# Kernel tuning notes

Measured on AMD Instinct MI355X. Metric: run time of the kernel, lower is better.

The kernel has to match this reference:

```python
import jax, jax.numpy as jnp
import numpy as np

D_MODEL = 1024
HEADS = 16
D_K = D_MODEL // HEADS


def setup_inputs() -> dict:
    key = jax.random.key(0)
    ks = jax.random.split(key, 12)
    B, S = 2, 2048
    scale = 1.0 / np.sqrt(D_MODEL)
    inp = {
        "q": jax.random.normal(ks[0], (B, S, D_MODEL), dtype=jnp.float32),
        "k": jax.random.normal(ks[1], (B, S, D_MODEL), dtype=jnp.float32),
        "v": jax.random.normal(ks[2], (B, S, D_MODEL), dtype=jnp.float32),
        "src_mask": jax.random.randint(ks[3], (B, 1, S), 0, 2, dtype=jnp.int32),
        # projection params (nn.Linear: y = x @ W.T + b); store W already transposed
        "Wq": jax.random.normal(ks[4], (D_MODEL, D_MODEL), dtype=jnp.float32) * scale,
        "bq": jnp.zeros((D_MODEL,), dtype=jnp.float32),
        "Wk": jax.random.normal(ks[5], (D_MODEL, D_MODEL), dtype=jnp.float32) * scale,
        "bk": jnp.zeros((D_MODEL,), dtype=jnp.float32),
        "Wv": jax.random.normal(ks[6], (D_MODEL, D_MODEL), dtype=jnp.float32) * scale,
        "bv": jnp.zeros((D_MODEL,), dtype=jnp.float32),
        "Wo": jax.random.normal(ks[7], (D_MODEL, D_MODEL), dtype=jnp.float32) * scale,
        "bo": jnp.zeros((D_MODEL,), dtype=jnp.float32),
    }
    return inp


def reference(q, k, v, src_mask, Wq, bq, Wk, bk, Wv, bv, Wo, bo):
    B, S, _ = q.shape
    # QKV projections, reshape to (b, heads, seq, d_k)
    def proj(x, W, b):
        y = x @ W + b  # (b, s, d_model)
        return y.reshape(B, S, HEADS, D_K).transpose(0, 2, 1, 3)

    qh = proj(q, Wq, bq)
    kh = proj(k, Wk, bk)
    vh = proj(v, Wv, bv)

    # scaled dot-product attention with padding mask
    scores = jnp.einsum("bhqd,bhkd->bhqk", qh, kh) / jnp.sqrt(jnp.float32(D_K))
    mask = src_mask[:, None, :, :]  # (b,1,1,s), broadcast over heads & query
    scores = jnp.where(mask == 0, jnp.float32(-1e9), scores)
    probs = jax.nn.softmax(scores, axis=-1)
    # dropout is identity in eval mode (reference baseline)
    ctx = jnp.einsum("bhqk,bhkd->bhqd", probs, vh)
    ctx = ctx.transpose(0, 2, 1, 3).reshape(B, S, D_MODEL)
    return ctx @ Wo + bo
```

## Files before the change

### kernel.cpp

```cpp
#include <hip/hip_runtime.h>
#include <hip/hip_bf16.h>

#define DM 1024
#define SL 2048
#define NH 16
#define DK 64

typedef __bf16 bf16;
typedef __bf16 bf16x8 __attribute__((ext_vector_type(8)));
typedef __bf16 bf16x4 __attribute__((ext_vector_type(4)));
typedef float f32x4 __attribute__((ext_vector_type(4)));
typedef float f32x16 __attribute__((ext_vector_type(16)));
typedef unsigned u32x4 __attribute__((ext_vector_type(4)));

__device__ __forceinline__ void gll16(const void* g, void* l) {
  __builtin_amdgcn_global_load_lds(
      (const __attribute__((address_space(1))) unsigned int*)g,
      (__attribute__((address_space(3))) unsigned int*)l, 16, 0, 0);
}

__device__ __forceinline__ unsigned pk2(float a, float b) {
  unsigned short lo = __builtin_bit_cast(unsigned short, (bf16)a);
  unsigned short hi = __builtin_bit_cast(unsigned short, (bf16)b);
  return (unsigned)lo | ((unsigned)hi << 16);
}

__global__ __launch_bounds__(256) void cvt_x_kernel(
    const float* __restrict__ q, const float* __restrict__ k, const float* __restrict__ v,
    bf16* __restrict__ xq, bf16* __restrict__ xk, bf16* __restrict__ xv) {
  const float* src; bf16* dst;
  if (blockIdx.y == 0)      { src = q; dst = xq; }
  else if (blockIdx.y == 1) { src = k; dst = xk; }
  else                      { src = v; dst = xv; }
  int i = (blockIdx.x * 256 + threadIdx.x) * 8;
  f32x4 a = *(const f32x4*)(src + i);
  f32x4 b = *(const f32x4*)(src + i + 4);
  bf16x8 o;
  o[0]=(bf16)a[0]; o[1]=(bf16)a[1]; o[2]=(bf16)a[2]; o[3]=(bf16)a[3];
  o[4]=(bf16)b[0]; o[5]=(bf16)b[1]; o[6]=(bf16)b[2]; o[7]=(bf16)b[3];
  *(bf16x8*)(dst + i) = o;
}

__global__ __launch_bounds__(256) void cvt_w_kernel(
    const float* __restrict__ W0, const float* __restrict__ W1,
    const float* __restrict__ W2, const float* __restrict__ W3,
    bf16* __restrict__ T0, bf16* __restrict__ T1,
    bf16* __restrict__ T2, bf16* __restrict__ T3) {
  const float* W; bf16* T;
  switch (blockIdx.y) {
    case 0:  W = W0; T = T0; break;
    case 1:  W = W1; T = T1; break;
    case 2:  W = W2; T = T2; break;
    default: W = W3; T = T3; break;
  }
  __shared__ float t[64][65];
  const int tid = threadIdx.x;
  const int tx = blockIdx.x & 15, ty = blockIdx.x >> 4;
  const int cr = tid >> 4, cc = tid & 15;
  #pragma unroll
  for (int rr = 0; rr < 4; ++rr) {
    int row = rr*16 + cr;
    f32x4 val = *(const f32x4*)(W + (ty*64 + row)*DM + tx*64 + cc*4);
    t[row][cc*4+0] = val[0]; t[row][cc*4+1] = val[1];
    t[row][cc*4+2] = val[2]; t[row][cc*4+3] = val[3];
  }
  __syncthreads();
  #pragma unroll
  for (int rr = 0; rr < 4; ++rr) {
    int nrow = rr*16 + cr;
    bf16x4 o;
    o[0] = (bf16)t[cc*4+0][nrow]; o[1] = (bf16)t[cc*4+1][nrow];
    o[2] = (bf16)t[cc*4+2][nrow]; o[3] = (bf16)t[cc*4+3][nrow];
    *(bf16x4*)(T + (tx*64 + nrow)*DM + ty*64 + cc*4) = o;
  }
}

template<int MODE>
__device__ __forceinline__ void gemm_core(
    const bf16* __restrict__ A, const bf16* __restrict__ Bt, const float* __restrict__ bias,
    bf16* __restrict__ outH, float* __restrict__ outF) {
  const int mt = blockIdx.x >> 3, nt = blockIdx.x & 7;
  const int m0 = mt*128, n0 = nt*128;
  __shared__ __attribute__((aligned(16))) bf16 As[128*64];
  __shared__ __attribute__((aligned(16))) bf16 Bs[128*64];
  const int tid = threadIdx.x, lane = tid & 63, w = tid >> 6;
  const int wm = w >> 1, wn = w & 1;
  f32x4 acc[4][4];
  #pragma unroll
  for (int x = 0; x < 4; ++x)
    #pragma unroll
    for (int y = 0; y < 4; ++y)
      #pragma unroll
      for (int e = 0; e < 4; ++e) acc[x][y][e] = 0.f;

  for (int kt = 0; kt < 16; ++kt) {
    const int k0 = kt*64;
    __syncthreads();
    #pragma unroll
    for (int i = 0; i < 4; ++i) {
      int idx = (i*4 + w)*64 + lane;
      int r = idx >> 3;
      int s = (idx & 7) ^ (r & 7);
      gll16(A  + (m0 + r)*DM + k0 + s*8, &As[(i*4 + w)*512]);
      gll16(Bt + (n0 + r)*DM + k0 + s*8, &Bs[(i*4 + w)*512]);
    }
    __syncthreads();
    bf16x8 bfr[4][2];
    #pragma unroll
    for (int ni = 0; ni < 4; ++ni) {
      int row = wn*64 + ni*16 + (lane & 15);
      #pragma unroll
      for (int c = 0; c < 2; ++c) {
        int slot = (lane >> 4) + c*4;
        bfr[ni][c] = *(const bf16x8*)&Bs[row*64 + ((slot ^ (row & 7)) << 3)];
      }
    }
    __builtin_amdgcn_s_setprio(1);
    #pragma unroll
    for (int mi = 0; mi < 4; ++mi) {
      int row = wm*64 + mi*16 + (lane & 15);
      bf16x8 a0 = *(const bf16x8*)&As[row*64 + ((((lane >> 4)    ) ^ (row & 7)) << 3)];
      bf16x8 a1 = *(const bf16x8*)&As[row*64 + ((((lane >> 4) + 4) ^ (row & 7)) << 3)];
      #pragma unroll
      for (int ni = 0; ni < 4; ++ni) {
        acc[mi][ni] = __builtin_amdgcn_mfma_f32_16x16x32_bf16(a0, bfr[ni][0], acc[mi][ni], 0, 0, 0);
        acc[mi][ni] = __builtin_amdgcn_mfma_f32_16x16x32_bf16(a1, bfr[ni][1], acc[mi][ni], 0, 0, 0);
      }
    }
    __builtin_amdgcn_s_setprio(0);
  }
  #pragma unroll
  for (int ni = 0; ni < 4; ++ni) {
    int n = n0 + wn*64 + ni*16 + (lane & 15);
    float bv = bias[n];
    #pragma unroll
    for (int mi = 0; mi < 4; ++mi) {
      int mb = m0 + wm*64 + mi*16 + ((lane >> 4) << 2);
      if (MODE == 2) {
        int bb = mb >> 11, ss = mb & 2047, hh = n >> 6, dd = n & 63;
        bf16x4 o;
        #pragma unroll
        for (int j = 0; j < 4; ++j) o[j] = (bf16)(acc[mi][ni][j] + bv);
        *(bf16x4*)&outH[(((bb << 4) + hh)*DK + dd)*SL + ss] = o;
      } else {
        #pragma unroll
        for (int j = 0; j < 4; ++j) {
          int m = mb + j;
          float val = acc[mi][ni][j] + bv;
          if (MODE == 1) {
            int bb = m >> 11, ss = m & 2047, hh = n >> 6, dd = n & 63;
            outH[(((bb << 4) + hh)*SL + ss)*DK + dd] = (bf16)val;
          } else {
            outF[m*DM + n] = val;
          }
        }
      }
    }
  }
}

__global__ __launch_bounds__(256, 2) void proj_gemm_kernel(
    const bf16* XQ, const bf16* XK, const bf16* XV,
    const bf16* WTQp, const bf16* WTKp, const bf16* WTVp,
    const float* bq, const float* bk, const float* bv,
    bf16* QHp, bf16* KHp, bf16* VTp) {
  if (blockIdx.y == 0)      gemm_core<1>(XQ, WTQp, bq, QHp, nullptr);
  else if (blockIdx.y == 1) gemm_core<1>(XK, WTKp, bk, KHp, nullptr);
  else                      gemm_core<2>(XV, WTVp, bv, VTp, nullptr);
}

__global__ __launch_bounds__(256, 2) void out_gemm_kernel(
    const bf16* CTXp, const bf16* WTOp, const float* bo, float* out) {
  gemm_core<0>(CTXp, WTOp, bo, nullptr, out);
}

__global__ __launch_bounds__(256, 2) void attn_kernel(
    const bf16* __restrict__ QHp, const bf16* __restrict__ KHp,
    const bf16* __restrict__ VTp, const int* __restrict__ msk,
    bf16* __restrict__ CTXp) {
  const int bh = blockIdx.y, b = bh >> 4, h = bh & 15;
  const int q0 = blockIdx.x * 128;
  const bf16* Qp  = QHp + bh * SL * DK;
  const bf16* Kp  = KHp + bh * SL * DK;
  const bf16* Vtp = VTp + bh * SL * DK;
  const int* mp = msk + b * SL;
  __shared__ __attribute__((aligned(16))) bf16 Ks[2][64*64];
  __shared__ __attribute__((aligned(16))) bf16 Vts[2][64*64];
  __shared__ __attribute__((aligned(16))) float mAddAll[SL];
  const int tid = threadIdx.x, lane = tid & 63, w = tid >> 6;
  const int hi = lane >> 5, l5 = lane & 31;
  const float L2E = 1.44269504f;

  #pragma unroll
  for (int i = 0; i < 8; ++i) {
    int idx = i*256 + tid;
    mAddAll[idx] = (mp[idx] == 0) ? -1.0e9f : 0.0f;
  }

  bf16x8 qf[4];
  {
    const bf16* qr = Qp + (q0 + w*32 + l5)*DK + hi*8;
    #pragma unroll
    for (int c = 0; c < 4; ++c) qf[c] = *(const bf16x8*)(qr + c*16);
  }
  f32x16 o0, o1;
  #pragma unroll
  for (int e = 0; e < 16; ++e) { o0[e] = 0.f; o1[e] = 0.f; }
  float m_run = -1e30f, l_run = 0.f;

  #define STAGE(buf, kt_)                                                  \
    {                                                                      \
      const int k0s = (kt_)*64;                                            \
      _Pragma("unroll")                                                    \
      for (int i = 0; i < 2; ++i) {                                        \
        int idx = (i*4 + w)*64 + lane;                                     \
        int r = idx >> 3;                                                  \
        int s = (idx & 7) ^ (r & 7);                                       \
        gll16(Kp + (k0s + r)*DK + s*8, &Ks[buf][(i*4 + w)*512]);           \
      }                                                                    \
      _Pragma("unroll")                                                    \
      for (int i = 0; i < 2; ++i) {                                        \
        int idx = (i*4 + w)*64 + lane;                                     \
        int r = idx >> 3;                                                  \
        int s = (idx & 7) ^ (r & 7);                                       \
        gll16(Vtp + r*SL + k0s + s*8, &Vts[buf][(i*4 + w)*512]);           \
      }                                                                    \
    }

  STAGE(0, 0);
  __syncthreads();

  for (int kt = 0; kt < 32; ++kt) {
    const int cur = kt & 1;
    const int k0 = kt*64;
    if (kt < 31) STAGE(cur ^ 1, kt + 1);

    f32x16 s0, s1;
    #pragma unroll
    for (int e = 0; e < 16; ++e) { s0[e] = 0.f; s1[e] = 0.f; }
    __builtin_amdgcn_s_setprio(1);
    #pragma unroll
    for (int c = 0; c < 4; ++c) {
      int sl = 2*c + hi;
      int r0 = l5, r1 = 32 + l5;
      bf16x8 kf0 = *(const bf16x8*)&Ks[cur][r0*64 + ((sl ^ (r0 & 7)) << 3)];
      bf16x8 kf1 = *(const bf16x8*)&Ks[cur][r1*64 + ((sl ^ (r1 & 7)) << 3)];
      s0 = __builtin_amdgcn_mfma_f32_32x32x16_bf16(kf0, qf[c], s0, 0, 0, 0);
      s1 = __builtin_amdgcn_mfma_f32_32x32x16_bf16(kf1, qf[c], s1, 0, 0, 0);
    }
    __builtin_amdgcn_s_setprio(0);

    float pv_[32];
    float mt = -1e30f;
    #pragma unroll
    for (int half = 0; half < 2; ++half) {
      #pragma unroll
      for (int qd = 0; qd < 4; ++qd) {
        f32x4 ma = *(const f32x4*)&mAddAll[k0 + half*32 + qd*8 + hi*4];
        #pragma unroll
        for (int j = 0; j < 4; ++j) {
          float val = (half ? s1[qd*4+j] : s0[qd*4+j]) * 0.125f + ma[j];
          pv_[half*16 + qd*4 + j] = val;
          mt = fmaxf(mt, val);
        }
      }
    }
    mt = fmaxf(mt, __shfl_xor(mt, 32));
    if (!__all(mt - m_run <= 8.0f)) {
      float mnew = fmaxf(m_run, mt);
      float sf = exp2f((m_run - mnew) * L2E);
      #pragma unroll
      for (int reg = 0; reg < 16; ++reg) {
        int crow = (reg & 3) + ((reg >> 2) << 3) + (hi << 2);
        float s_ = __shfl(sf, crow);
        o0[reg] *= s_; o1[reg] *= s_;
      }
      l_run *= sf;
      m_run = mnew;
    }
    float lsum = 0.f;
    #pragma unroll
    for (int t = 0; t < 32; ++t) {
      float p = exp2f((pv_[t] - m_run) * L2E);
      pv_[t] = p; lsum += p;
    }
    lsum += __shfl_xor(lsum, 32);
    l_run += lsum;

    #pragma unroll
    for (int c = 0; c < 4; ++c) {
      const int half_c = c >> 1;
      const int iA = half_c*16 + (((2*c)    ) & 3)*4;
      const int iB = half_c*16 + (((2*c) + 1) & 3)*4;
      unsigned wA0 = pk2(pv_[iA],   pv_[iA+1]);
      unsigned wA1 = pk2(pv_[iA+2], pv_[iA+3]);
      unsigned wB0 = pk2(pv_[iB],   pv_[iB+1]);
      unsigned wB1 = pk2(pv_[iB+2], pv_[iB+3]);
      unsigned ow0 = hi ? wB0 : wA0, ow1 = hi ? wB1 : wA1;
      unsigned xw0 = hi ? wA0 : wB0, xw1 = hi ? wA1 : wB1;
      unsigned yw0 = __shfl_xor(xw0, 32);
      unsigned yw1 = __shfl_xor(xw1, 32);
      u32x4 uu;
      uu[0] = hi ? yw0 : ow0;
      uu[1] = hi ? yw1 : ow1;
      uu[2] = hi ? ow0 : yw0;
      uu[3] = hi ? ow1 : yw1;
      bf16x8 pa = __builtin_bit_cast(bf16x8, uu);
      int sl = 2*c + hi;
      int r0 = l5, r1 = 32 + l5;
      bf16x8 vf0 = *(const bf16x8*)&Vts[cur][r0*64 + ((sl ^ (r0 & 7)) << 3)];
      bf16x8 vf1 = *(const bf16x8*)&Vts[cur][r1*64 + ((sl ^ (r1 & 7)) << 3)];
      __builtin_amdgcn_s_setprio(1);
      o0 = __builtin_amdgcn_mfma_f32_32x32x16_bf16(pa, vf0, o0, 0, 0, 0);
      o1 = __builtin_amdgcn_mfma_f32_32x32x16_bf16(pa, vf1, o1, 0, 0, 0);
      __builtin_amdgcn_s_setprio(0);
    }
    __syncthreads();
  }

  float inv = 1.f / l_run;
  const int sbase = (b * SL) * DM + h * DK;
  #pragma unroll
  for (int reg = 0; reg < 16; ++reg) {
    int crow = (reg & 3) + ((reg >> 2) << 3) + (hi << 2);
    float iv = __shfl(inv, crow);
    int srow = q0 + w*32 + crow;
    CTXp[sbase + srow*DM + l5]      = (bf16)(o0[reg] * iv);
    CTXp[sbase + srow*DM + 32 + l5] = (bf16)(o1[reg] * iv);
  }
  #undef STAGE
}

extern "C" void kernel_launch(void* const* d_in, const int* in_sizes, int n_in,
                              void* d_out, int out_size, void* d_ws, size_t ws_size,
                              hipStream_t stream) {
  const float* q  = (const float*)d_in[0];
  const float* k  = (const float*)d_in[1];
  const float* v  = (const float*)d_in[2];
  const int*  msk = (const int*)d_in[3];
  const float* Wq = (const float*)d_in[4];
  const float* bq = (const float*)d_in[5];
  const float* Wk = (const float*)d_in[6];
  const float* bk = (const float*)d_in[7];
  const float* Wv = (const float*)d_in[8];
  const float* bv = (const float*)d_in[9];
  const float* Wo = (const float*)d_in[10];
  const float* bo = (const float*)d_in[11];
  char* ws = (char*)d_ws;
  bf16* XQ  = (bf16*)(ws + 0);
  bf16* XK  = (bf16*)(ws + 8388608);
  bf16* XV  = (bf16*)(ws + 16777216);
  bf16* WTQ = (bf16*)(ws + 25165824);
  bf16* WTK = (bf16*)(ws + 27262976);
  bf16* WTV = (bf16*)(ws + 29360128);
  bf16* WTO = (bf16*)(ws + 31457280);
  bf16* QHb = (bf16*)(ws + 33554432);
  bf16* KHb = (bf16*)(ws + 41943040);
  bf16* VTb = (bf16*)(ws + 50331648);
  bf16* CTX = (bf16*)(ws + 58720256);
  float* out = (float*)d_out;

  cvt_x_kernel<<<dim3(2048, 3), 256, 0, stream>>>(q, k, v, XQ, XK, XV);
  cvt_w_kernel<<<dim3(256, 4), 256, 0, stream>>>(Wq, Wk, Wv, Wo, WTQ, WTK, WTV, WTO);
  proj_gemm_kernel<<<dim3(256, 3), 256, 0, stream>>>(XQ, XK, XV, WTQ, WTK, WTV,
                                                     bq, bk, bv, QHb, KHb, VTb);
  attn_kernel<<<dim3(16, 32), 256, 0, stream>>>(QHb, KHb, VTb, msk, CTX);
  out_gemm_kernel<<<dim3(256, 1), 256, 0, stream>>>(CTX, WTO, bo, out);
}
```

Before: 269.3 us.

## Shrink GEMM tiles, swizzle block order, precompute mask bias, fold log2e scaling

The projection and output GEMMs go from 128x128 to 64x128 tiles with an XCD-aware block swizzle and higher occupancy bounds, doubling the grid. Attention gets a flat grid remapped so each XCD handles whole heads, and reads a precomputed float mask bias (pre-scaled by log2e) from a small new kernel instead of building it in LDS. The scale and log2e are folded into one multiply, the rescale threshold is raised to match, and the max/sum reductions are split into four independent chains for ILP. The mask bias reuses workspace that XQ occupies, which is safe only because XQ is no longer needed once the projection kernel has finished.

```diff
diff --git a/kernel.cpp b/kernel.cpp
--- a/kernel.cpp
+++ b/kernel.cpp
@@ -75,19 +75,33 @@
   }
 }
 
+__global__ __launch_bounds__(256) void maskcvt_kernel(
+    const int* __restrict__ msk, float* __restrict__ mBias) {
+  int i = (blockIdx.x * 256 + threadIdx.x) * 4;
+  int4 m4 = *(const int4*)(msk + i);
+  f32x4 o;
+  o[0] = (m4.x == 0) ? -1.4426950e9f : 0.f;
+  o[1] = (m4.y == 0) ? -1.4426950e9f : 0.f;
+  o[2] = (m4.z == 0) ? -1.4426950e9f : 0.f;
+  o[3] = (m4.w == 0) ? -1.4426950e9f : 0.f;
+  *(f32x4*)(mBias + i) = o;
+}
+
 template<int MODE>
 __device__ __forceinline__ void gemm_core(
     const bf16* __restrict__ A, const bf16* __restrict__ Bt, const float* __restrict__ bias,
     bf16* __restrict__ outH, float* __restrict__ outF) {
-  const int mt = blockIdx.x >> 3, nt = blockIdx.x & 7;
-  const int m0 = mt*128, n0 = nt*128;
-  __shared__ __attribute__((aligned(16))) bf16 As[128*64];
+  const int bid = blockIdx.x;
+  const int swz = (bid & 7) * 64 + (bid >> 3);
+  const int mt = swz >> 3, nt = swz & 7;
+  const int m0 = mt*64, n0 = nt*128;
+  __shared__ __attribute__((aligned(16))) bf16 As[64*64];
   __shared__ __attribute__((aligned(16))) bf16 Bs[128*64];
   const int tid = threadIdx.x, lane = tid & 63, w = tid >> 6;
   const int wm = w >> 1, wn = w & 1;
-  f32x4 acc[4][4];
-  #pragma unroll
-  for (int x = 0; x < 4; ++x)
+  f32x4 acc[2][4];
+  #pragma unroll
+  for (int x = 0; x < 2; ++x)
     #pragma unroll
     for (int y = 0; y < 4; ++y)
       #pragma unroll
@@ -96,12 +110,18 @@
   for (int kt = 0; kt < 16; ++kt) {
     const int k0 = kt*64;
     __syncthreads();
+    #pragma unroll
+    for (int i = 0; i < 2; ++i) {
+      int idx = (i*4 + w)*64 + lane;
+      int r = idx >> 3;
+      int s = (idx & 7) ^ (r & 7);
+      gll16(A + (m0 + r)*DM + k0 + s*8, &As[(i*4 + w)*512]);
+    }
     #pragma unroll
     for (int i = 0; i < 4; ++i) {
       int idx = (i*4 + w)*64 + lane;
       int r = idx >> 3;
       int s = (idx & 7) ^ (r & 7);
-      gll16(A  + (m0 + r)*DM + k0 + s*8, &As[(i*4 + w)*512]);
       gll16(Bt + (n0 + r)*DM + k0 + s*8, &Bs[(i*4 + w)*512]);
     }
     __syncthreads();
@@ -117,8 +137,8 @@
     }
     __builtin_amdgcn_s_setprio(1);
     #pragma unroll
-    for (int mi = 0; mi < 4; ++mi) {
-      int row = wm*64 + mi*16 + (lane & 15);
+    for (int mi = 0; mi < 2; ++mi) {
+      int row = wm*32 + mi*16 + (lane & 15);
       bf16x8 a0 = *(const bf16x8*)&As[row*64 + ((((lane >> 4)    ) ^ (row & 7)) << 3)];
       bf16x8 a1 = *(const bf16x8*)&As[row*64 + ((((lane >> 4) + 4) ^ (row & 7)) << 3)];
       #pragma unroll
@@ -134,8 +154,8 @@
     int n = n0 + wn*64 + ni*16 + (lane & 15);
     float bv = bias[n];
     #pragma unroll
-    for (int mi = 0; mi < 4; ++mi) {
-      int mb = m0 + wm*64 + mi*16 + ((lane >> 4) << 2);
+    for (int mi = 0; mi < 2; ++mi) {
+      int mb = m0 + wm*32 + mi*16 + ((lane >> 4) << 2);
       if (MODE == 2) {
         int bb = mb >> 11, ss = mb & 2047, hh = n >> 6, dd = n & 63;
         bf16x4 o;
@@ -159,7 +179,7 @@
   }
 }
 
-__global__ __launch_bounds__(256, 2) void proj_gemm_kernel(
+__global__ __launch_bounds__(256, 4) void proj_gemm_kernel(
     const bf16* XQ, const bf16* XK, const bf16* XV,
     const bf16* WTQp, const bf16* WTKp, const bf16* WTVp,
     const float* bq, const float* bk, const float* bv,
@@ -169,33 +189,30 @@
   else                      gemm_core<2>(XV, WTVp, bv, VTp, nullptr);
 }
 
-__global__ __launch_bounds__(256, 2) void out_gemm_kernel(
+__global__ __launch_bounds__(256, 4) void out_gemm_kernel(
     const bf16* CTXp, const bf16* WTOp, const float* bo, float* out) {
   gemm_core<0>(CTXp, WTOp, bo, nullptr, out);
 }
 
 __global__ __launch_bounds__(256, 2) void attn_kernel(
     const bf16* __restrict__ QHp, const bf16* __restrict__ KHp,
-    const bf16* __restrict__ VTp, const int* __restrict__ msk,
+    const bf16* __restrict__ VTp, const float* __restrict__ mBias,
     bf16* __restrict__ CTXp) {
-  const int bh = blockIdx.y, b = bh >> 4, h = bh & 15;
-  const int q0 = blockIdx.x * 128;
+  const int d = blockIdx.x;
+  const int xcd = d & 7, rr = d >> 3;
+  const int bh = xcd*4 + (rr >> 4);
+  const int qt = rr & 15;
+  const int b = bh >> 4, h = bh & 15;
+  const int q0 = qt * 128;
   const bf16* Qp  = QHp + bh * SL * DK;
   const bf16* Kp  = KHp + bh * SL * DK;
   const bf16* Vtp = VTp + bh * SL * DK;
-  const int* mp = msk + b * SL;
+  const float* mb_ = mBias + b * SL;
   __shared__ __attribute__((aligned(16))) bf16 Ks[2][64*64];
   __shared__ __attribute__((aligned(16))) bf16 Vts[2][64*64];
-  __shared__ __attribute__((aligned(16))) float mAddAll[SL];
   const int tid = threadIdx.x, lane = tid & 63, w = tid >> 6;
   const int hi = lane >> 5, l5 = lane & 31;
-  const float L2E = 1.44269504f;
-
-  #pragma unroll
-  for (int i = 0; i < 8; ++i) {
-    int idx = i*256 + tid;
-    mAddAll[idx] = (mp[idx] == 0) ? -1.0e9f : 0.0f;
-  }
+  const float SCL2E = 0.18033688f;
 
   bf16x8 qf[4];
   {
@@ -233,6 +250,14 @@
   for (int kt = 0; kt < 32; ++kt) {
     const int cur = kt & 1;
     const int k0 = kt*64;
+
+    f32x4 mreg[2][4];
+    #pragma unroll
+    for (int half = 0; half < 2; ++half)
+      #pragma unroll
+      for (int qd = 0; qd < 4; ++qd)
+        mreg[half][qd] = *(const f32x4*)&mb_[k0 + half*32 + qd*8 + hi*4];
+
     if (kt < 31) STAGE(cur ^ 1, kt + 1);
 
     f32x16 s0, s1;
@@ -251,24 +276,28 @@
     __builtin_amdgcn_s_setprio(0);
 
     float pv_[32];
-    float mt = -1e30f;
+    float mtv0 = -1e30f, mtv1 = -1e30f, mtv2 = -1e30f, mtv3 = -1e30f;
     #pragma unroll
     for (int half = 0; half < 2; ++half) {
       #pragma unroll
       for (int qd = 0; qd < 4; ++qd) {
-        f32x4 ma = *(const f32x4*)&mAddAll[k0 + half*32 + qd*8 + hi*4];
+        f32x4 ma = mreg[half][qd];
         #pragma unroll
         for (int j = 0; j < 4; ++j) {
-          float val = (half ? s1[qd*4+j] : s0[qd*4+j]) * 0.125f + ma[j];
+          float val = (half ? s1[qd*4+j] : s0[qd*4+j]) * SCL2E + ma[j];
           pv_[half*16 + qd*4 + j] = val;
-          mt = fmaxf(mt, val);
+          if (j == 0) mtv0 = fmaxf(mtv0, val);
+          else if (j == 1) mtv1 = fmaxf(mtv1, val);
+          else if (j == 2) mtv2 = fmaxf(mtv2, val);
+          else mtv3 = fmaxf(mtv3, val);
         }
       }
     }
+    float mt = fmaxf(fmaxf(mtv0, mtv1), fmaxf(mtv2, mtv3));
     mt = fmaxf(mt, __shfl_xor(mt, 32));
-    if (!__all(mt - m_run <= 8.0f)) {
+    if (!__all(mt - m_run <= 11.5f)) {
       float mnew = fmaxf(m_run, mt);
-      float sf = exp2f((m_run - mnew) * L2E);
+      float sf = exp2f(m_run - mnew);
       #pragma unroll
       for (int reg = 0; reg < 16; ++reg) {
         int crow = (reg & 3) + ((reg >> 2) << 3) + (hi << 2);
@@ -278,12 +307,17 @@
       l_run *= sf;
       m_run = mnew;
     }
-    float lsum = 0.f;
+    float ls0 = 0.f, ls1 = 0.f, ls2 = 0.f, ls3 = 0.f;
     #pragma unroll
     for (int t = 0; t < 32; ++t) {
-      float p = exp2f((pv_[t] - m_run) * L2E);
-      pv_[t] = p; lsum += p;
-    }
+      float p = exp2f(pv_[t] - m_run);
+      pv_[t] = p;
+      if ((t & 3) == 0) ls0 += p;
+      else if ((t & 3) == 1) ls1 += p;
+      else if ((t & 3) == 2) ls2 += p;
+      else ls3 += p;
+    }
+    float lsum = (ls0 + ls1) + (ls2 + ls3);
     lsum += __shfl_xor(lsum, 32);
     l_run += lsum;
 
@@ -358,12 +392,14 @@
   bf16* KHb = (bf16*)(ws + 41943040);
   bf16* VTb = (bf16*)(ws + 50331648);
   bf16* CTX = (bf16*)(ws + 58720256);
+  float* mBias = (float*)(ws + 0);
   float* out = (float*)d_out;
 
   cvt_x_kernel<<<dim3(2048, 3), 256, 0, stream>>>(q, k, v, XQ, XK, XV);
   cvt_w_kernel<<<dim3(256, 4), 256, 0, stream>>>(Wq, Wk, Wv, Wo, WTQ, WTK, WTV, WTO);
-  proj_gemm_kernel<<<dim3(256, 3), 256, 0, stream>>>(XQ, XK, XV, WTQ, WTK, WTV,
+  proj_gemm_kernel<<<dim3(512, 3), 256, 0, stream>>>(XQ, XK, XV, WTQ, WTK, WTV,
                                                      bq, bk, bv, QHb, KHb, VTb);
-  attn_kernel<<<dim3(16, 32), 256, 0, stream>>>(QHb, KHb, VTb, msk, CTX);
-  out_gemm_kernel<<<dim3(256, 1), 256, 0, stream>>>(CTX, WTO, bo, out);
-}
+  maskcvt_kernel<<<dim3(4), 256, 0, stream>>>(msk, mBias);
+  attn_kernel<<<dim3(512), 256, 0, stream>>>(QHb, KHb, VTb, mBias, CTX);
+  out_gemm_kernel<<<dim3(512), 256, 0, stream>>>(CTX, WTO, bo, out);
+}
```

New measurement: 258.4 us. -4.0%, faster.
